# Kernel optimization log

Measured on AMD Instinct MI355X. Metric: run time of the kernel, lower is better.

Reference implementation:

```python
import jax, jax.numpy as jnp
import numpy as np

N, D, C, T = 4096, 1024, 1000, 32  # tokens, n_embd, n_class, n_logit_samples


def setup_inputs() -> dict:
    key = jax.random.key(0)
    k1, k2 = jax.random.split(key)
    x = jax.random.normal(k1, (N, D), dtype=jnp.float32)
    # 0.02 init scale keeps exp(logvar) numerically sane (standard GPT-style init)
    W = jax.random.normal(k2, (2 * C, D), dtype=jnp.float32) * 0.02
    return {"x": x, "W": W}


def reference(x, W):
    # linear head (bias-free): [N, D] @ [D, 2C] -> [N, 2C]
    h = jnp.einsum('nd,cd->nc', x, W)
    mu, logvar = h[:, :C], h[:, C:]
    sigma = jnp.exp(0.5 * logvar)  # sqrt(exp(logvar))

    # MC sampling of logits, vectorized over the T sample loop.
    # torch subtracts the row max before softmax; that is exactly what a
    # numerically-stable softmax does, so the math is identical.
    eps = jax.random.normal(jax.random.key(42), (T, N, C), dtype=mu.dtype)
    logits = mu[None] + sigma[None] * eps           # [T, N, C]
    probs = jax.nn.softmax(logits, axis=-1)         # [T, N, C]
    prob = jnp.mean(probs, axis=0)                  # [N, C]
    mu_out = jnp.exp(prob)                          # faithful to torch.exp(prob)
    return (mu_out, sigma)
```

## Files before the change

### kernel.cpp

```cpp
#include <hip/hip_runtime.h>


typedef __attribute__((ext_vector_type(8))) _Float16 f16x8;
typedef __attribute__((ext_vector_type(4))) float f32x4;
typedef __attribute__((ext_vector_type(2))) float f32x2;

#define NC_TOT  4096000
#define H_HALF  65536000u

__device__ __forceinline__ unsigned short f2h(float f) {
  _Float16 h = (_Float16)f;
  return __builtin_bit_cast(unsigned short, h);
}

__global__ __launch_bounds__(256) void convert_kernel(
    const float* __restrict__ x, const float* __restrict__ W,
    unsigned short* __restrict__ xh, unsigned short* __restrict__ wh) {
  int qid = blockIdx.x * 256 + threadIdx.x;
  if (qid < 1048576) {
    float4 v = ((const float4*)x)[qid];
    ((ushort4*)xh)[qid] = make_ushort4(f2h(v.x), f2h(v.y), f2h(v.z), f2h(v.w));
  } else {
    int q = qid - 1048576;
    int row = q >> 8;
    ushort4 o;
    if (row < 2000) {
      float4 v = ((const float4*)W)[q];
      o = make_ushort4(f2h(v.x), f2h(v.y), f2h(v.z), f2h(v.w));
    } else {
      o = make_ushort4(0, 0, 0, 0);
    }
    ((ushort4*)wh)[q] = o;
  }
}

#define BK 32

typedef __attribute__((address_space(3))) unsigned char lds_byte;
typedef __attribute__((address_space(1))) unsigned char glb_byte;

__device__ __forceinline__ void glds16(const unsigned short* g, unsigned short* l) {
  __builtin_amdgcn_global_load_lds((const glb_byte*)g, (lds_byte*)l, 16, 0, 0);
}

__global__ __launch_bounds__(256) void gemm_kernel(
    const unsigned short* __restrict__ Ah,
    const unsigned short* __restrict__ Bh,
    float* __restrict__ mu,
    float* __restrict__ sigma_out) {
  const int K = 1024;
  __shared__ unsigned short As[128 * BK];
  __shared__ unsigned short Bs[64 * BK];

  int id  = blockIdx.x;
  int xcd = id & 7;
  int q9  = id >> 3;
  int by  = xcd * 4 + (q9 >> 5);
  int bx  = q9 & 31;

  int tid  = threadIdx.x;
  int w    = tid >> 6;
  int lane = tid & 63;
  int wr   = (w >> 1) * 64;
  int wc   = (w & 1) * 32;
  int lrow = lane & 15;
  int kq   = lane >> 4;

  f32x4 acc[4][2];
  for (int i = 0; i < 4; i++)
    for (int j = 0; j < 2; j++) acc[i][j] = (f32x4){0.f, 0.f, 0.f, 0.f};

  int srow = w * 16 + (lane >> 2);
  int scol = (lane & 3) * 8;
  const unsigned short* Ap = Ah + (by * 128 + srow) * K + scol;
  const unsigned short* Bp = Bh + (bx * 64  + srow) * K + scol;
  unsigned short* lA = As + w * 512;
  unsigned short* lB = Bs + w * 512;

  for (int kk = 0; kk < K; kk += BK) {
    __syncthreads();
    glds16(Ap + kk,          lA);
    glds16(Ap + kk + 64 * K, lA + 2048);
    glds16(Bp + kk,          lB);
    __syncthreads();

    f16x8 a[4], b[2];
    for (int i = 0; i < 4; i++)
      a[i] = *(const f16x8*)(As + (wr + i * 16 + lrow) * BK + kq * 8);
    for (int j = 0; j < 2; j++)
      b[j] = *(const f16x8*)(Bs + (wc + j * 16 + lrow) * BK + kq * 8);
    for (int i = 0; i < 4; i++)
      for (int j = 0; j < 2; j++)
        acc[i][j] = __builtin_amdgcn_mfma_f32_16x16x32_f16(a[i], b[j], acc[i][j], 0, 0, 0);
  }

  int orow0 = by * 128 + wr + (lane >> 4) * 4;
  int ocol0 = bx * 64 + wc + (lane & 15);
  for (int i = 0; i < 4; i++) {
    for (int j = 0; j < 2; j++) {
      int c = ocol0 + j * 16;
      for (int v = 0; v < 4; v++) {
        int r = orow0 + i * 16 + v;
        float val = acc[i][j][v];
        if (c < 1000)       mu[r * 1000 + c] = val;
        else if (c < 2000)  sigma_out[r * 1000 + (c - 1000)] = __expf(0.5f * val);
      }
    }
  }
}

__device__ __forceinline__ unsigned rotl_(unsigned x, unsigned r) {
  return __builtin_amdgcn_alignbit(x, x, 32u - r);
}

__device__ __forceinline__ void threefry(unsigned x0, unsigned x1,
                                         unsigned& o0, unsigned& o1) {
  const unsigned ks1 = 42u;
  const unsigned ks2 = 0x1BD11BDAu ^ 42u;
#define TF_RND(r) { x0 += x1; x1 = rotl_(x1, r); x1 ^= x0; }
  x1 += ks1;
  TF_RND(13) TF_RND(15) TF_RND(26) TF_RND(6)
  x0 += ks1;  x1 += ks2 + 1u;
  TF_RND(17) TF_RND(29) TF_RND(16) TF_RND(24)
  x0 += ks2;  x1 += 2u;
  TF_RND(13) TF_RND(15) TF_RND(26) TF_RND(6)
  x1 += ks1 + 3u;
  TF_RND(17) TF_RND(29) TF_RND(16) TF_RND(24)
  x0 += ks1;  x1 += ks2 + 4u;
  TF_RND(13) TF_RND(15) TF_RND(26) TF_RND(6)
  x0 += ks2;  x1 += 5u;
#undef TF_RND
  o0 = x0; o1 = x1;
}

__device__ __forceinline__ f32x2 splat2(float c) { return (f32x2){c, c}; }

__device__ __forceinline__ float erfinv_big_p(float x, float lg) {
  float w = lg * -0.69314718f;
  float v = __fsqrt_rn(w) - 3.0f;
  float p = -0.000200214257f;
  p = fmaf(p, v, 0.000100950558f);
  p = fmaf(p, v, 0.00134934322f);
  p = fmaf(p, v, -0.00367342844f);
  p = fmaf(p, v, 0.00573950773f);
  p = fmaf(p, v, -0.0076224613f);
  p = fmaf(p, v, 0.00943887047f);
  p = fmaf(p, v, 1.00167406f);
  p = fmaf(p, v, 2.83297682f);
  return p * x;
}

__device__ __forceinline__ f32x2 normal2p(f32x2 x) {
  f32x2 t = __builtin_elementwise_fma(-x, x, splat2(1.0f));
  f32x2 lg;
  lg.x = __builtin_amdgcn_logf(t.x);
  lg.y = __builtin_amdgcn_logf(t.y);
  f32x2 v = __builtin_elementwise_fma(lg, splat2(-0.69314718f), splat2(-2.5f));
  f32x2 p = splat2(2.81022636e-08f);
  p = __builtin_elementwise_fma(p, v, splat2(3.43273939e-07f));
  p = __builtin_elementwise_fma(p, v, splat2(-3.5233877e-06f));
  p = __builtin_elementwise_fma(p, v, splat2(-4.39150654e-06f));
  p = __builtin_elementwise_fma(p, v, splat2(0.00021858087f));
  p = __builtin_elementwise_fma(p, v, splat2(-0.00125372503f));
  p = __builtin_elementwise_fma(p, v, splat2(-0.00417768164f));
  p = __builtin_elementwise_fma(p, v, splat2(0.246640727f));
  p = __builtin_elementwise_fma(p, v, splat2(1.50140941f));
  f32x2 r = p * x;
  bool c0 = lg.x <= -7.2134752f;
  bool c1 = lg.y <= -7.2134752f;
  if (__builtin_expect(__ballot(c0 || c1) != 0ull, false)) {
    if (c0) r.x = erfinv_big_p(x.x, lg.x);
    if (c1) r.y = erfinv_big_p(x.y, lg.y);
  }
  return r;
}

__device__ __forceinline__ f32x2 bits_to_u2(unsigned b0, unsigned b1) {
  f32x2 f;
  f.x = __builtin_bit_cast(float, (b0 >> 9) | 0x3f800000u);
  f.y = __builtin_bit_cast(float, (b1 >> 9) | 0x3f800000u);
  f = f - splat2(1.0f);
  return __builtin_elementwise_fma(f, splat2(2.0f), splat2(-0.99999994f));
}

__global__ __launch_bounds__(256, 2) void sample_kernel(
    const float* __restrict__ mu,
    const float* __restrict__ sigma,
    float* __restrict__ out0) {
  int n    = blockIdx.x;
  int tid  = threadIdx.x;
  int lane = tid & 63, w = tid >> 6;
  __shared__ float pbuf[4][1024];

  const float L2E    = 1.44269504f;
  const float SQ2L2E = 1.41421356f * 1.44269504f;

  int cb = n * 1000;
  float mu2[16], sg2[16], prob[16];
#pragma unroll
  for (int j = 0; j < 16; j++) {
    int c = j * 64 + lane;
    bool val = (c < 1000);
    mu2[j]  = val ? mu[cb + c] * L2E       : -1e30f;
    sg2[j]  = val ? sigma[cb + c] * SQ2L2E : 0.f;
    prob[j] = 0.f;
  }

  f32x2 e[16];
#pragma unroll 1
  for (int it = 0; it < 4; it++) {
    int t = w * 4 + it;
    unsigned ib = (unsigned)(t * 4096000 + cb) + (unsigned)lane;
    f32x2 s = splat2(0.f);
#pragma unroll
    for (int j = 0; j < 16; j++) {
      unsigned i0 = ib + (unsigned)(j * 64);
      unsigned o0, o1;
      threefry(i0, i0 + H_HALF, o0, o1);
      f32x2 epsp = normal2p(bits_to_u2(o0, o1));
      float ex = __builtin_amdgcn_exp2f(fmaf(sg2[j], epsp.x, mu2[j]));
      float ey = __builtin_amdgcn_exp2f(fmaf(sg2[j], epsp.y, mu2[j]));
      asm volatile("" : "+v"(ex), "+v"(ey));
      e[j] = (f32x2){ex, ey};
      s.x += ex;
      s.y += ey;
    }
#pragma unroll
    for (int m = 1; m < 64; m <<= 1) {
      s.x += __shfl_xor(s.x, m, 64);
      s.y += __shfl_xor(s.y, m, 64);
    }
    float rA = __builtin_amdgcn_rcpf(s.x);
    float rB = __builtin_amdgcn_rcpf(s.y);
#pragma unroll
    for (int j = 0; j < 16; j++)
      prob[j] = fmaf(e[j].x, rA, fmaf(e[j].y, rB, prob[j]));
  }

#pragma unroll
  for (int j = 0; j < 16; j++)
    pbuf[w][j * 64 + lane] = prob[j];
  __syncthreads();
#pragma unroll
  for (int k = 0; k < 4; k++) {
    int c = tid + k * 256;
    if (c < 1000) {
      float sm = pbuf[0][c] + pbuf[1][c] + pbuf[2][c] + pbuf[3][c];
      out0[cb + c] = __builtin_amdgcn_exp2f(sm * (0.03125f * 1.44269504f));
    }
  }
}

extern "C" void kernel_launch(void* const* d_in, const int* in_sizes, int n_in,
                              void* d_out, int out_size, void* d_ws, size_t ws_size,
                              hipStream_t stream) {
  const float* x = (const float*)d_in[0];
  const float* W = (const float*)d_in[1];
  float* out = (float*)d_out;

  unsigned short* xh = (unsigned short*)d_ws;
  unsigned short* wh = (unsigned short*)((char*)d_ws + 8388608);
  float*          mu = (float*)((char*)d_ws + 12582912);
  float* sigma = out + NC_TOT;

  convert_kernel<<<6144, 256, 0, stream>>>(x, W, xh, wh);
  gemm_kernel<<<1024, 256, 0, stream>>>(xh, wh, mu, sigma);
  sample_kernel<<<4096, 256, 0, stream>>>(mu, sigma, out);
}
```

Before: 281.6 us.

## Precompute first quarter of Gaussian samples in interleaved GEMM blocks

The GEMM launch doubles its grid so odd blocks generate the threefry normal samples for the first sample iteration of each wave and store them to workspace, overlapping RNG compute with the memory/MFMA-bound GEMM. The sample kernel then loads those precomputed eps values for iteration zero instead of regenerating them. It costs a 128 MB workspace write and read and only activates when the workspace is large enough.

```diff
diff --git a/kernel.cpp b/kernel.cpp
--- a/kernel.cpp
+++ b/kernel.cpp
@@ -7,6 +7,8 @@
 
 #define NC_TOT  4096000
 #define H_HALF  65536000u
+#define EPS2_OFF 28966912u
+#define WS_NEED  163184640u
 
 __device__ __forceinline__ unsigned short f2h(float f) {
   _Float16 h = (_Float16)f;
@@ -31,81 +33,6 @@
       o = make_ushort4(0, 0, 0, 0);
     }
     ((ushort4*)wh)[q] = o;
-  }
-}
-
-#define BK 32
-
-typedef __attribute__((address_space(3))) unsigned char lds_byte;
-typedef __attribute__((address_space(1))) unsigned char glb_byte;
-
-__device__ __forceinline__ void glds16(const unsigned short* g, unsigned short* l) {
-  __builtin_amdgcn_global_load_lds((const glb_byte*)g, (lds_byte*)l, 16, 0, 0);
-}
-
-__global__ __launch_bounds__(256) void gemm_kernel(
-    const unsigned short* __restrict__ Ah,
-    const unsigned short* __restrict__ Bh,
-    float* __restrict__ mu,
-    float* __restrict__ sigma_out) {
-  const int K = 1024;
-  __shared__ unsigned short As[128 * BK];
-  __shared__ unsigned short Bs[64 * BK];
-
-  int id  = blockIdx.x;
-  int xcd = id & 7;
-  int q9  = id >> 3;
-  int by  = xcd * 4 + (q9 >> 5);
-  int bx  = q9 & 31;
-
-  int tid  = threadIdx.x;
-  int w    = tid >> 6;
-  int lane = tid & 63;
-  int wr   = (w >> 1) * 64;
-  int wc   = (w & 1) * 32;
-  int lrow = lane & 15;
-  int kq   = lane >> 4;
-
-  f32x4 acc[4][2];
-  for (int i = 0; i < 4; i++)
-    for (int j = 0; j < 2; j++) acc[i][j] = (f32x4){0.f, 0.f, 0.f, 0.f};
-
-  int srow = w * 16 + (lane >> 2);
-  int scol = (lane & 3) * 8;
-  const unsigned short* Ap = Ah + (by * 128 + srow) * K + scol;
-  const unsigned short* Bp = Bh + (bx * 64  + srow) * K + scol;
-  unsigned short* lA = As + w * 512;
-  unsigned short* lB = Bs + w * 512;
-
-  for (int kk = 0; kk < K; kk += BK) {
-    __syncthreads();
-    glds16(Ap + kk,          lA);
-    glds16(Ap + kk + 64 * K, lA + 2048);
-    glds16(Bp + kk,          lB);
-    __syncthreads();
-
-    f16x8 a[4], b[2];
-    for (int i = 0; i < 4; i++)
-      a[i] = *(const f16x8*)(As + (wr + i * 16 + lrow) * BK + kq * 8);
-    for (int j = 0; j < 2; j++)
-      b[j] = *(const f16x8*)(Bs + (wc + j * 16 + lrow) * BK + kq * 8);
-    for (int i = 0; i < 4; i++)
-      for (int j = 0; j < 2; j++)
-        acc[i][j] = __builtin_amdgcn_mfma_f32_16x16x32_f16(a[i], b[j], acc[i][j], 0, 0, 0);
-  }
-
-  int orow0 = by * 128 + wr + (lane >> 4) * 4;
-  int ocol0 = bx * 64 + wc + (lane & 15);
-  for (int i = 0; i < 4; i++) {
-    for (int j = 0; j < 2; j++) {
-      int c = ocol0 + j * 16;
-      for (int v = 0; v < 4; v++) {
-        int r = orow0 + i * 16 + v;
-        float val = acc[i][j][v];
-        if (c < 1000)       mu[r * 1000 + c] = val;
-        else if (c < 2000)  sigma_out[r * 1000 + (c - 1000)] = __expf(0.5f * val);
-      }
-    }
   }
 }
 
@@ -183,10 +110,113 @@
   return __builtin_elementwise_fma(f, splat2(2.0f), splat2(-0.99999994f));
 }
 
+#define BK 32
+
+typedef __attribute__((address_space(3))) unsigned char lds_byte;
+typedef __attribute__((address_space(1))) unsigned char glb_byte;
+
+__device__ __forceinline__ void glds16(const unsigned short* g, unsigned short* l) {
+  __builtin_amdgcn_global_load_lds((const glb_byte*)g, (lds_byte*)l, 16, 0, 0);
+}
+
+__global__ __launch_bounds__(256) void gemm_rng_kernel(
+    const unsigned short* __restrict__ Ah,
+    const unsigned short* __restrict__ Bh,
+    float* __restrict__ mu,
+    float* __restrict__ sigma_out,
+    f32x2* __restrict__ eps2,
+    int pre) {
+  const int K = 1024;
+  __shared__ unsigned short As[128 * BK];
+  __shared__ unsigned short Bs[64 * BK];
+
+  int bid = blockIdx.x;
+  int id;  bool rng;
+  if (pre) { rng = (bid & 1) != 0; id = bid >> 1; }
+  else     { rng = false;          id = bid;      }
+
+  int tid  = threadIdx.x;
+  int w    = tid >> 6;
+  int lane = tid & 63;
+
+  if (rng) {
+    for (int k = 0; k < 4; k++) {
+      int n  = id * 4 + k;
+      int cb = n * 1000;
+      unsigned ib = (unsigned)((w * 4) * 4096000 + cb) + (unsigned)lane;
+      f32x2* base = eps2 + (w * 4096 + n) * 1024 + lane;
+#pragma unroll
+      for (int j = 0; j < 16; j++) {
+        unsigned i0 = ib + (unsigned)(j * 64);
+        unsigned o0, o1;
+        threefry(i0, i0 + H_HALF, o0, o1);
+        f32x2 epsp = normal2p(bits_to_u2(o0, o1));
+        unsigned long long bits = __builtin_bit_cast(unsigned long long, epsp);
+        __builtin_nontemporal_store(bits, (unsigned long long*)(base + j * 64));
+      }
+    }
+    return;
+  }
+
+  int xcd = id & 7;
+  int q9  = id >> 3;
+  int by  = xcd * 4 + (q9 >> 5);
+  int bx  = q9 & 31;
+
+  int wr   = (w >> 1) * 64;
+  int wc   = (w & 1) * 32;
+  int lrow = lane & 15;
+  int kq   = lane >> 4;
+
+  f32x4 acc[4][2];
+  for (int i = 0; i < 4; i++)
+    for (int j = 0; j < 2; j++) acc[i][j] = (f32x4){0.f, 0.f, 0.f, 0.f};
+
+  int srow = w * 16 + (lane >> 2);
+  int scol = (lane & 3) * 8;
+  const unsigned short* Ap = Ah + (by * 128 + srow) * K + scol;
+  const unsigned short* Bp = Bh + (bx * 64  + srow) * K + scol;
+  unsigned short* lA = As + w * 512;
+  unsigned short* lB = Bs + w * 512;
+
+  for (int kk = 0; kk < K; kk += BK) {
+    __syncthreads();
+    glds16(Ap + kk,          lA);
+    glds16(Ap + kk + 64 * K, lA + 2048);
+    glds16(Bp + kk,          lB);
+    __syncthreads();
+
+    f16x8 a[4], b[2];
+    for (int i = 0; i < 4; i++)
+      a[i] = *(const f16x8*)(As + (wr + i * 16 + lrow) * BK + kq * 8);
+    for (int j = 0; j < 2; j++)
+      b[j] = *(const f16x8*)(Bs + (wc + j * 16 + lrow) * BK + kq * 8);
+    for (int i = 0; i < 4; i++)
+      for (int j = 0; j < 2; j++)
+        acc[i][j] = __builtin_amdgcn_mfma_f32_16x16x32_f16(a[i], b[j], acc[i][j], 0, 0, 0);
+  }
+
+  int orow0 = by * 128 + wr + (lane >> 4) * 4;
+  int ocol0 = bx * 64 + wc + (lane & 15);
+  for (int i = 0; i < 4; i++) {
+    for (int j = 0; j < 2; j++) {
+      int c = ocol0 + j * 16;
+      for (int v = 0; v < 4; v++) {
+        int r = orow0 + i * 16 + v;
+        float val = acc[i][j][v];
+        if (c < 1000)       mu[r * 1000 + c] = val;
+        else if (c < 2000)  sigma_out[r * 1000 + (c - 1000)] = __expf(0.5f * val);
+      }
+    }
+  }
+}
+
 __global__ __launch_bounds__(256, 2) void sample_kernel(
     const float* __restrict__ mu,
     const float* __restrict__ sigma,
-    float* __restrict__ out0) {
+    float* __restrict__ out0,
+    const f32x2* __restrict__ eps2,
+    int pre) {
   int n    = blockIdx.x;
   int tid  = threadIdx.x;
   int lane = tid & 63, w = tid >> 6;
@@ -206,24 +236,39 @@
     prob[j] = 0.f;
   }
 
+  const f32x2* epb = eps2 + (w * 4096 + n) * 1024 + lane;
+
   f32x2 e[16];
 #pragma unroll 1
   for (int it = 0; it < 4; it++) {
     int t = w * 4 + it;
     unsigned ib = (unsigned)(t * 4096000 + cb) + (unsigned)lane;
     f32x2 s = splat2(0.f);
-#pragma unroll
-    for (int j = 0; j < 16; j++) {
-      unsigned i0 = ib + (unsigned)(j * 64);
-      unsigned o0, o1;
-      threefry(i0, i0 + H_HALF, o0, o1);
-      f32x2 epsp = normal2p(bits_to_u2(o0, o1));
-      float ex = __builtin_amdgcn_exp2f(fmaf(sg2[j], epsp.x, mu2[j]));
-      float ey = __builtin_amdgcn_exp2f(fmaf(sg2[j], epsp.y, mu2[j]));
-      asm volatile("" : "+v"(ex), "+v"(ey));
-      e[j] = (f32x2){ex, ey};
-      s.x += ex;
-      s.y += ey;
+    if (it == 0 && pre) {
+#pragma unroll
+      for (int j = 0; j < 16; j++) {
+        f32x2 epsp = epb[j * 64];
+        float ex = __builtin_amdgcn_exp2f(fmaf(sg2[j], epsp.x, mu2[j]));
+        float ey = __builtin_amdgcn_exp2f(fmaf(sg2[j], epsp.y, mu2[j]));
+        asm volatile("" : "+v"(ex), "+v"(ey));
+        e[j] = (f32x2){ex, ey};
+        s.x += ex;
+        s.y += ey;
+      }
+    } else {
+#pragma unroll
+      for (int j = 0; j < 16; j++) {
+        unsigned i0 = ib + (unsigned)(j * 64);
+        unsigned o0, o1;
+        threefry(i0, i0 + H_HALF, o0, o1);
+        f32x2 epsp = normal2p(bits_to_u2(o0, o1));
+        float ex = __builtin_amdgcn_exp2f(fmaf(sg2[j], epsp.x, mu2[j]));
+        float ey = __builtin_amdgcn_exp2f(fmaf(sg2[j], epsp.y, mu2[j]));
+        asm volatile("" : "+v"(ex), "+v"(ey));
+        e[j] = (f32x2){ex, ey};
+        s.x += ex;
+        s.y += ey;
+      }
     }
 #pragma unroll
     for (int m = 1; m < 64; m <<= 1) {
@@ -261,9 +306,12 @@
   unsigned short* xh = (unsigned short*)d_ws;
   unsigned short* wh = (unsigned short*)((char*)d_ws + 8388608);
   float*          mu = (float*)((char*)d_ws + 12582912);
+  f32x2*        eps2 = (f32x2*)((char*)d_ws + EPS2_OFF);
   float* sigma = out + NC_TOT;
 
+  int pre = (ws_size >= (size_t)WS_NEED) ? 1 : 0;
+
   convert_kernel<<<6144, 256, 0, stream>>>(x, W, xh, wh);
-  gemm_kernel<<<1024, 256, 0, stream>>>(xh, wh, mu, sigma);
-  sample_kernel<<<4096, 256, 0, stream>>>(mu, sigma, out);
-}
+  gemm_rng_kernel<<<1024 * (1 + pre), 256, 0, stream>>>(xh, wh, mu, sigma, eps2, pre);
+  sample_kernel<<<4096, 256, 0, stream>>>(mu, sigma, out, eps2, pre);
+}
```

Result: slower. 309.9 us (+10.1%).
